# Kernel tuning notes

Measured on AMD Instinct MI355X. Metric: run time of the kernel, lower is better.

Reference implementation:

```python
import jax, jax.numpy as jnp
import numpy as np

N_NODES = 100_000
N_EDGES = 1_000_000
N_GRAPHS = 2048
F_IN, N_HEADS, HEAD_DIM = 128, 2, 32
NEG_SLOPE = 0.2


def seg_softmax(logits, seg, num):
    # numerically stable scatter-softmax over segments (leading axis)
    m = jax.ops.segment_max(logits, seg, num_segments=num)
    e = jnp.exp(logits - m[seg])
    s = jax.ops.segment_sum(e, seg, num_segments=num)
    return e / s[seg]


def setup_inputs() -> dict:
    key = jax.random.key(0)
    ks = jax.random.split(key, 10)
    HC = N_HEADS * HEAD_DIM
    x = jax.random.normal(ks[0], (N_NODES, F_IN), jnp.float32)
    edge_index = jax.random.randint(ks[1], (2, N_EDGES), 0, N_NODES, jnp.int32)
    batch = jnp.sort(jax.random.randint(ks[2], (N_NODES,), 0, N_GRAPHS, jnp.int32))
    sc_in = 1.0 / np.sqrt(F_IN)
    sc_hc = 1.0 / np.sqrt(HC)
    W_l = jax.random.normal(ks[3], (F_IN, HC), jnp.float32) * sc_in
    W_r = jax.random.normal(ks[4], (F_IN, HC), jnp.float32) * sc_in
    att = jax.random.normal(ks[5], (N_HEADS, HEAD_DIM), jnp.float32) * (1.0 / np.sqrt(HEAD_DIM))
    bias = jnp.zeros((HC,), jnp.float32)
    w_rel = jax.random.normal(ks[6], (HC,), jnp.float32) * sc_hc
    w_root = jax.random.normal(ks[7], (HC,), jnp.float32) * sc_hc
    b_score = jnp.zeros((1,), jnp.float32)
    return {"x": x, "edge_index": edge_index, "batch": batch, "W_l": W_l,
            "W_r": W_r, "att": att, "bias": bias, "w_rel": w_rel,
            "w_root": w_root, "b_score": b_score}


def reference(x, edge_index, batch, W_l, W_r, att, bias, w_rel, w_root, b_score):
    N = x.shape[0]
    H, C = att.shape
    src, dst = edge_index[0], edge_index[1]
    # --- GATv2Conv (add_self_loops=True, concat heads, negative_slope=0.2) ---
    loop = jnp.arange(N, dtype=src.dtype)
    s = jnp.concatenate([src, loop])  # source j
    d = jnp.concatenate([dst, loop])  # target i
    xl = (x @ W_l).reshape(N, H, C)   # lin_l -> source features
    xr = (x @ W_r).reshape(N, H, C)   # lin_r -> target features
    e = jax.nn.leaky_relu(xl[s] + xr[d], NEG_SLOPE)       # [E', H, C]
    logits = jnp.einsum('ehc,hc->eh', e, att)              # [E', H]
    alpha = seg_softmax(logits, d, N)                      # softmax over incoming edges per target
    h = jax.ops.segment_sum(xl[s] * alpha[:, :, None], d, num_segments=N)
    h = h.reshape(N, H * C) + bias                         # conv output (data.x)
    # --- SAGPooling(min_score=-1): softmax(GraphConv score) keeps all nodes ---
    aggr = jax.ops.segment_sum(h[src], dst, num_segments=N)  # GraphConv neighbor add-aggr
    score = aggr @ w_rel + h @ w_root + b_score              # [N]
    sm = seg_softmax(score, batch, N_GRAPHS)
    px = h * sm[:, None]
    # --- global_add_pool + global_mean_pool ---
    add = jax.ops.segment_sum(px, batch, num_segments=N_GRAPHS)
    cnt = jax.ops.segment_sum(jnp.ones((N,), px.dtype), batch, num_segments=N_GRAPHS)
    mean = add / jnp.maximum(cnt, 1.0)[:, None]
    return add + mean  # global_emb [N_GRAPHS, H*C]
```

## Files before the change

kernel.cpp:

```cpp
#include <hip/hip_runtime.h>
#include <hip/hip_bf16.h>

#define N_NODES 100000
#define N_EDGES 1000000
#define N_GRAPHS 2048
#define F_IN 128
#define NEG_SLOPE 0.2f
#define E_TOT (N_EDGES + N_NODES)
#define GEMM_BLOCKS 782
#define NODE_BLOCKS 391
#define NB 1563
#define EB 269
#define EB_PAD 272
#define CPW_BLOCKS 391

typedef short  bf16x8 __attribute__((ext_vector_type(8)));
typedef float  f32x16 __attribute__((ext_vector_type(16)));

__device__ __forceinline__ short f2bf(float f) {
    unsigned u = __float_as_uint(f);
    unsigned r = (u + 0x7fffu + ((u >> 16) & 1u)) >> 16;
    return (short)r;
}
__device__ __forceinline__ float bf2f(short h) {
    return __uint_as_float(((unsigned)(unsigned short)h) << 16);
}

template <int CTRL>
__device__ __forceinline__ float dpp_add(float x) {
    return x + __int_as_float(__builtin_amdgcn_update_dpp(
        0, __float_as_int(x), CTRL, 0xf, 0xf, true));
}
__device__ __forceinline__ float head_sum_bcast(float x) {
    x = dpp_add<0x111>(x);
    x = dpp_add<0x112>(x);
    x = dpp_add<0x114>(x);
    x = dpp_add<0x118>(x);
    x = dpp_add<0x142>(x);
    return __int_as_float(__builtin_amdgcn_ds_swizzle(__float_as_int(x), 0x03E0));
}
__device__ __forceinline__ float full_sum64(float x) {
    x = dpp_add<0x111>(x);
    x = dpp_add<0x112>(x);
    x = dpp_add<0x114>(x);
    x = dpp_add<0x118>(x);
    x = dpp_add<0x142>(x);
    x = dpp_add<0x143>(x);
    return x;
}
__device__ __forceinline__ float quad_sum(float x) {
    x = dpp_add<0xB1>(x);
    x = dpp_add<0x4E>(x);
    return x;
}

__global__ __launch_bounds__(256) void k_gemm_bhist(const float* __restrict__ x,
                                                    const float* __restrict__ Wl,
                                                    const float* __restrict__ Wr,
                                                    const int* __restrict__ ei,
                                                    float* __restrict__ xlr,
                                                    int* __restrict__ bhist) {
    __shared__ unsigned char smem[2 * 128 * 136 * 2];
    int tid = threadIdx.x;
    if (blockIdx.x >= GEMM_BLOCKS) {
        int* lh = (int*)smem;
        int b = blockIdx.x - GEMM_BLOCKS;
        for (int i = tid; i < NB; i += 256) lh[i] = 0;
        __syncthreads();
        int e0 = b * 4096;
#pragma unroll
        for (int j = 0; j < 16; ++j) {
            int e = e0 + j * 256 + tid;
            if (e < E_TOT) {
                int d = (e < N_EDGES) ? ei[N_EDGES + e] : (e - N_EDGES);
                atomicAdd(&lh[d >> 6], 1);
            }
        }
        __syncthreads();
        for (int i = tid; i < NB; i += 256)
            bhist[(size_t)i * EB_PAD + b] = lh[i];
        return;
    }
    typedef short wt_t[128][136];
    wt_t* wt = (wt_t*)smem;
    {
        int k  = tid >> 1;
        int cq = tid & 1;
        const float* Wsrc = cq ? Wr : Wl;
#pragma unroll
        for (int u = 0; u < 16; ++u) {
            int c0 = u * 4;
            float4 wv = *(const float4*)(Wsrc + (size_t)k * 64 + c0);
            float vv[4] = {wv.x, wv.y, wv.z, wv.w};
#pragma unroll
            for (int q = 0; q < 4; ++q) {
                int c = cq * 64 + c0 + q;
                short hi = f2bf(vv[q]);
                wt[0][c][k] = hi;
                wt[1][c][k] = f2bf(vv[q] - bf2f(hi));
            }
        }
    }
    __syncthreads();
    int lane = tid & 63, w = tid >> 6;
    int m = lane & 31, half = lane >> 5;
    int row = blockIdx.x * 128 + w * 32 + m;
    bool rv = row < N_NODES;
    const float* xrow = x + (size_t)(rv ? row : 0) * F_IN;
    f32x16 acc[4];
#pragma unroll
    for (int t = 0; t < 4; ++t)
#pragma unroll
        for (int i = 0; i < 16; ++i) acc[t][i] = 0.f;

#pragma unroll
    for (int kt = 0; kt < 8; ++kt) {
        int kb = kt * 16 + half * 8;
        float4 xa = rv ? *(const float4*)(xrow + kb)
                       : make_float4(0.f, 0.f, 0.f, 0.f);
        float4 xb = rv ? *(const float4*)(xrow + kb + 4)
                       : make_float4(0.f, 0.f, 0.f, 0.f);
        float xs[8] = {xa.x, xa.y, xa.z, xa.w, xb.x, xb.y, xb.z, xb.w};
        bf16x8 ahi, alo;
#pragma unroll
        for (int j = 0; j < 8; ++j) {
            short hi = f2bf(xs[j]);
            ahi[j] = hi;
            alo[j] = f2bf(xs[j] - bf2f(hi));
        }
#pragma unroll
        for (int t = 0; t < 4; ++t) {
            int n = t * 32 + m;
            bf16x8 bhi = *(const bf16x8*)&wt[0][n][kb];
            bf16x8 blo = *(const bf16x8*)&wt[1][n][kb];
            acc[t] = __builtin_amdgcn_mfma_f32_32x32x16_bf16(ahi, bhi, acc[t], 0, 0, 0);
            acc[t] = __builtin_amdgcn_mfma_f32_32x32x16_bf16(ahi, blo, acc[t], 0, 0, 0);
            acc[t] = __builtin_amdgcn_mfma_f32_32x32x16_bf16(alo, bhi, acc[t], 0, 0, 0);
        }
    }
    int r0 = blockIdx.x * 128 + w * 32 + 4 * half;
#pragma unroll
    for (int t = 0; t < 4; ++t)
#pragma unroll
        for (int reg = 0; reg < 16; ++reg) {
            int rr = r0 + (reg & 3) + 8 * (reg >> 2);
            if (rr < N_NODES)
                xlr[(size_t)rr * 128 + t * 32 + m] = acc[t][reg];
        }
}

__global__ __launch_bounds__(256) void k_colprefix_bounds(int* __restrict__ bhist,
                                                          int* __restrict__ colsum,
                                                          const int* __restrict__ batch,
                                                          int* __restrict__ start) {
    if (blockIdx.x < CPW_BLOCKS) {
        int wv = blockIdx.x * 4 + (threadIdx.x >> 6);
        if (wv >= NB) return;
        int lane = threadIdx.x & 63;
        int* row = bhist + (size_t)wv * EB_PAD;
        int carry = 0;
        for (int base = 0; base < EB; base += 64) {
            int idx = base + lane;
            int v = (idx < EB) ? row[idx] : 0;
            int inc = v;
#pragma unroll
            for (int o = 1; o < 64; o <<= 1) {
                int t = __shfl_up(inc, o, 64);
                if (lane >= o) inc += t;
            }
            int tot = __shfl(inc, 63, 64);
            if (idx < EB) row[idx] = carry + inc - v;
            carry += tot;
        }
        if (lane == 0) colsum[wv] = carry;
    } else {
        int i = (blockIdx.x - CPW_BLOCKS) * 256 + threadIdx.x;
        if (i >= N_NODES) return;
        int bi = batch[i];
        int bp = (i == 0) ? -1 : batch[i - 1];
        for (int g = bp + 1; g <= bi; ++g) start[g] = i;
        if (i == N_NODES - 1)
            for (int g = bi + 1; g <= N_GRAPHS; ++g) start[g] = N_NODES;
    }
}

__global__ __launch_bounds__(256) void k_bscatter(const int* __restrict__ ei,
                                                  const int* __restrict__ bhist,
                                                  const int* __restrict__ colsum,
                                                  int* __restrict__ colbase,
                                                  int* __restrict__ bpack) {
    __shared__ int lh[NB];
    __shared__ int cb[NB + 1];
    __shared__ int sctmp[256];
    int tid = threadIdx.x, b = blockIdx.x;
    {
        int v[7]; int s = 0;
#pragma unroll
        for (int k = 0; k < 7; ++k) {
            int idx = tid * 7 + k;
            v[k] = (idx < NB) ? colsum[idx] : 0;
            s += v[k];
        }
        sctmp[tid] = s; __syncthreads();
        for (int off = 1; off < 256; off <<= 1) {
            int xv = (tid >= off) ? sctmp[tid - off] : 0;
            __syncthreads();
            sctmp[tid] += xv;
            __syncthreads();
        }
        int run = sctmp[tid] - s;
#pragma unroll
        for (int k = 0; k < 7; ++k) {
            int idx = tid * 7 + k;
            if (idx <= NB) cb[idx] = run;
            run += v[k];
        }
    }
    for (int i = tid; i < NB; i += 256) lh[i] = 0;
    __syncthreads();
    if (b == 0)
        for (int i = tid; i <= NB; i += 256) colbase[i] = cb[i];
    int e0 = b * 4096;
#pragma unroll
    for (int j = 0; j < 16; ++j) {
        int e = e0 + j * 256 + tid;
        if (e < E_TOT) {
            int s, d;
            if (e < N_EDGES) { s = ei[e]; d = ei[N_EDGES + e]; }
            else             { s = d = e - N_EDGES; }
            int bk = d >> 6;
            int lr = atomicAdd(&lh[bk], 1);
            int pos = cb[bk] + bhist[(size_t)bk * EB_PAD + b] + lr;
            bpack[pos] = s | ((d & 63) << 17);
        }
    }
}

__global__ __launch_bounds__(256) void k_fine(const int* __restrict__ bpack,
                                              const int* __restrict__ colbase,
                                              int* __restrict__ rowptr,
                                              int* __restrict__ sorted_src) {
    __shared__ int fcnt[64];
    __shared__ int foff[64];
    int i = blockIdx.x, tid = threadIdx.x;
    int cb0 = colbase[i], cb1 = colbase[i + 1];
    if (tid < 64) fcnt[tid] = 0;
    __syncthreads();
    for (int e = cb0 + tid; e < cb1; e += 256)
        atomicAdd(&fcnt[bpack[e] >> 17], 1);
    __syncthreads();
    if (tid < 64) {
        int v = fcnt[tid];
        int inc = v;
#pragma unroll
        for (int o = 1; o < 64; o <<= 1) {
            int t = __shfl_up(inc, o, 64);
            if (tid >= o) inc += t;
        }
        int excl = inc - v;
        foff[tid] = excl;
        int node = i * 64 + tid;
        if (node <= N_NODES) rowptr[node] = cb0 + excl;
    }
    __syncthreads();
    for (int e = cb0 + tid; e < cb1; e += 256) {
        int w = bpack[e];
        int lr = atomicAdd(&foff[w >> 17], 1);
        sorted_src[cb0 + lr] = w & 131071;
    }
}

__global__ __launch_bounds__(256) void k_gat(const float* __restrict__ xlr,
                                             const int* __restrict__ rowptr,
                                             const int* __restrict__ sorted_src,
                                             const float* __restrict__ att,
                                             const float* __restrict__ bias,
                                             const float* __restrict__ w_rel,
                                             const float* __restrict__ w_root,
                                             float* __restrict__ hfeat,
                                             float* __restrict__ tbuf,
                                             float* __restrict__ rbuf) {
    int lane = threadIdx.x & 63;
    int du = __builtin_amdgcn_readfirstlane(blockIdx.x * 4 + (threadIdx.x >> 6));
    if (du >= N_NODES) return;
    float xr_l  = xlr[(size_t)du * 128 + 64 + lane];
    float att_l = att[lane];
    int j0 = __builtin_amdgcn_readfirstlane(rowptr[du]);
    int j1 = __builtin_amdgcn_readfirstlane(rowptr[du + 1]);
    float wsum = 0.f, acc = 0.f;
    int jc = j0;
    float xv[8];
    {
        int jj = jc + (lane & 7);
        if (jj > j1 - 1) jj = j1 - 1;
        int sv = sorted_src[jj];
#pragma unroll
        for (int i = 0; i < 8; ++i) {
            int s = __builtin_amdgcn_readlane(sv, i);
            xv[i] = (xlr + (size_t)(unsigned)s * 128)[lane];
        }
    }
    while (true) {
        int n = j1 - jc;
        int jn = jc + 8;
        bool more = jn < j1;
        float xvn[8];
        if (more) {
            int jj = jn + (lane & 7);
            if (jj > j1 - 1) jj = j1 - 1;
            int sv = sorted_src[jj];
#pragma unroll
            for (int i = 0; i < 8; ++i) {
                int s = __builtin_amdgcn_readlane(sv, i);
                xvn[i] = (xlr + (size_t)(unsigned)s * 128)[lane];
            }
        }
        float p[8];
#pragma unroll
        for (int i = 0; i < 8; ++i) {
            float v = xv[i] + xr_l;
            v = (v > 0.f) ? v : NEG_SLOPE * v;
            p[i] = v * att_l;
        }
#pragma unroll
        for (int i = 0; i < 8; ++i)
            p[i] = head_sum_bcast(p[i]);
        if (n >= 8) {
#pragma unroll
            for (int i = 0; i < 8; ++i) {
                float w = __expf(p[i]);
                wsum += w;
                acc += w * xv[i];
            }
        } else {
#pragma unroll
            for (int i = 0; i < 8; ++i) {
                float w = (i < n) ? __expf(p[i]) : 0.f;
                wsum += w;
                acc += w * xv[i];
            }
        }
        if (!more) break;
        jc = jn;
#pragma unroll
        for (int i = 0; i < 8; ++i) xv[i] = xvn[i];
    }
    float h = acc / wsum + bias[lane];
    hfeat[(size_t)du * 64 + lane] = h;
    float a = full_sum64(h * w_rel[lane]);
    float b = full_sum64(h * w_root[lane]);
    if (lane == 63) { tbuf[du] = a; rbuf[du] = b; }
}

__global__ __launch_bounds__(256) void k_pool(const int* __restrict__ rowptr,
                                              const int* __restrict__ sorted_src,
                                              const float* __restrict__ t,
                                              const float* __restrict__ r,
                                              const float* __restrict__ b_score,
                                              float* __restrict__ score,
                                              const float* __restrict__ h,
                                              const int* __restrict__ start,
                                              float* __restrict__ out) {
    __shared__ float sh[4];
    __shared__ float shacc[4][64];
    int g = blockIdx.x;
    int tid = threadIdx.x, w = tid >> 6, lane = tid & 63;
    int n0 = start[g], n1 = start[g + 1];
    int cnt = n1 - n0;
    if (cnt <= 0) { if (tid < 64) out[(size_t)g * 64 + tid] = 0.f; return; }
    float bsc = b_score[0];
    for (int base = n0; base < n1; base += 64) {
        int i = base + (tid >> 2);
        float sum = 0.f;
        int jj0 = 0, jj1 = 0;
        if (i < n1) { jj0 = rowptr[i]; jj1 = rowptr[i + 1]; }
        for (int j = jj0 + (tid & 3); j < jj1; j += 4)
            sum += t[sorted_src[j]];
        sum = quad_sum(sum);
        if (i < n1 && (tid & 3) == 0)
            score[i] = sum - t[i] + r[i] + bsc;
    }
    __syncthreads();
    float m = -1e30f;
    for (int i = n0 + tid; i < n1; i += 256) m = fmaxf(m, score[i]);
#pragma unroll
    for (int o = 32; o; o >>= 1) m = fmaxf(m, __shfl_xor(m, o, 64));
    if (lane == 0) sh[w] = m;
    __syncthreads();
    m = fmaxf(fmaxf(sh[0], sh[1]), fmaxf(sh[2], sh[3]));
    __syncthreads();
    float ssum = 0.f;
    for (int i = n0 + tid; i < n1; i += 256) {
        float e = __expf(score[i] - m);
        score[i] = e;
        ssum += e;
    }
#pragma unroll
    for (int o = 32; o; o >>= 1) ssum += __shfl_xor(ssum, o, 64);
    if (lane == 0) sh[w] = ssum;
    __syncthreads();
    ssum = sh[0] + sh[1] + sh[2] + sh[3];
    float acc = 0.f;
    for (int i = n0 + w; i < n1; i += 4)
        acc += score[i] * h[(size_t)i * 64 + lane];
    shacc[w][lane] = acc;
    __syncthreads();
    if (w == 0) {
        float tot = shacc[0][lane] + shacc[1][lane] + shacc[2][lane] + shacc[3][lane];
        out[(size_t)g * 64 + lane] = tot * (1.f + 1.f / (float)cnt) / ssum;
    }
}

extern "C" void kernel_launch(void* const* d_in, const int* in_sizes, int n_in,
                              void* d_out, int out_size, void* d_ws, size_t ws_size,
                              hipStream_t stream) {
    const float* x      = (const float*)d_in[0];
    const int*   ei     = (const int*)d_in[1];
    const int*   batch  = (const int*)d_in[2];
    const float* Wl     = (const float*)d_in[3];
    const float* Wr     = (const float*)d_in[4];
    const float* att    = (const float*)d_in[5];
    const float* bias   = (const float*)d_in[6];
    const float* w_rel  = (const float*)d_in[7];
    const float* w_root = (const float*)d_in[8];
    const float* b_sc   = (const float*)d_in[9];

    char* ws = (char*)d_ws;
    size_t off = 0;
    auto alloc = [&](size_t bytes) { void* p = ws + off; off += (bytes + 255) & ~255ull; return p; };
    float* xlr        = (float*)alloc((size_t)N_NODES * 128 * 4);
    float* hfeat      = (float*)alloc((size_t)N_NODES * 64 * 4);
    int*   bhist      = (int*)hfeat;
    int*   bpack      = (int*)  alloc((size_t)E_TOT * 4);
    int*   sorted_src = (int*)  alloc((size_t)E_TOT * 4);
    int*   rowptr     = (int*)  alloc((size_t)(N_NODES + 1) * 4);
    int*   colsum     = (int*)  alloc((size_t)NB * 4);
    int*   colbase    = (int*)  alloc((size_t)(NB + 1) * 4);
    float* tbuf       = (float*)alloc((size_t)N_NODES * 4);
    float* rbuf       = (float*)alloc((size_t)N_NODES * 4);
    float* score      = (float*)alloc((size_t)N_NODES * 4);
    int*   start      = (int*)  alloc((size_t)(N_GRAPHS + 1) * 4);

    k_gemm_bhist      <<<GEMM_BLOCKS + EB, 256, 0, stream>>>(x, Wl, Wr, ei, xlr, bhist);
    k_colprefix_bounds<<<CPW_BLOCKS + NODE_BLOCKS, 256, 0, stream>>>(bhist, colsum, batch, start);
    k_bscatter        <<<EB, 256, 0, stream>>>(ei, bhist, colsum, colbase, bpack);
    k_fine            <<<NB, 256, 0, stream>>>(bpack, colbase, rowptr, sorted_src);
    k_gat             <<<(N_NODES + 3) / 4, 256, 0, stream>>>(xlr, rowptr, sorted_src, att, bias,
                                                              w_rel, w_root, hfeat, tbuf, rbuf);
    k_pool            <<<N_GRAPHS, 256, 0, stream>>>(rowptr, sorted_src, tbuf, rbuf, b_sc,
                                                     score, hfeat, start, (float*)d_out);
}
```

Measured before the change: 238.0 us.

## Store source features in bf16 and process 8 edges per wave in parallel lanes

Measured after the change: 229.8 us. 3.4% less time.

```diff
diff --git a/kernel.cpp b/kernel.cpp
--- a/kernel.cpp
+++ b/kernel.cpp
@@ -31,14 +31,6 @@
     return x + __int_as_float(__builtin_amdgcn_update_dpp(
         0, __float_as_int(x), CTRL, 0xf, 0xf, true));
 }
-__device__ __forceinline__ float head_sum_bcast(float x) {
-    x = dpp_add<0x111>(x);
-    x = dpp_add<0x112>(x);
-    x = dpp_add<0x114>(x);
-    x = dpp_add<0x118>(x);
-    x = dpp_add<0x142>(x);
-    return __int_as_float(__builtin_amdgcn_ds_swizzle(__float_as_int(x), 0x03E0));
-}
 __device__ __forceinline__ float full_sum64(float x) {
     x = dpp_add<0x111>(x);
     x = dpp_add<0x112>(x);
@@ -58,7 +50,8 @@
                                                     const float* __restrict__ Wl,
                                                     const float* __restrict__ Wr,
                                                     const int* __restrict__ ei,
-                                                    float* __restrict__ xlr,
+                                                    float* __restrict__ xr,
+                                                    short* __restrict__ xlb,
                                                     int* __restrict__ bhist) {
     __shared__ unsigned char smem[2 * 128 * 136 * 2];
     int tid = threadIdx.x;
@@ -144,8 +137,12 @@
 #pragma unroll
         for (int reg = 0; reg < 16; ++reg) {
             int rr = r0 + (reg & 3) + 8 * (reg >> 2);
-            if (rr < N_NODES)
-                xlr[(size_t)rr * 128 + t * 32 + m] = acc[t][reg];
+            if (rr < N_NODES) {
+                if (t < 2)
+                    xlb[(size_t)rr * 64 + t * 32 + m] = f2bf(acc[t][reg]);
+                else
+                    xr[(size_t)rr * 64 + (t - 2) * 32 + m] = acc[t][reg];
+            }
         }
 }
 
@@ -270,7 +267,8 @@
     }
 }
 
-__global__ __launch_bounds__(256) void k_gat(const float* __restrict__ xlr,
+__global__ __launch_bounds__(256) void k_gat(const short* __restrict__ xlb,
+                                             const float* __restrict__ xr,
                                              const int* __restrict__ rowptr,
                                              const int* __restrict__ sorted_src,
                                              const float* __restrict__ att,
@@ -283,72 +281,72 @@
     int lane = threadIdx.x & 63;
     int du = __builtin_amdgcn_readfirstlane(blockIdx.x * 4 + (threadIdx.x >> 6));
     if (du >= N_NODES) return;
-    float xr_l  = xlr[(size_t)du * 128 + 64 + lane];
-    float att_l = att[lane];
+    int grp = lane >> 3, sub = lane & 7;
+    float xr8[8], att8[8];
+    {
+        float4 a = *(const float4*)(xr + (size_t)du * 64 + sub * 8);
+        float4 b = *(const float4*)(xr + (size_t)du * 64 + sub * 8 + 4);
+        xr8[0]=a.x; xr8[1]=a.y; xr8[2]=a.z; xr8[3]=a.w;
+        xr8[4]=b.x; xr8[5]=b.y; xr8[6]=b.z; xr8[7]=b.w;
+        float4 c = *(const float4*)(att + sub * 8);
+        float4 d = *(const float4*)(att + sub * 8 + 4);
+        att8[0]=c.x; att8[1]=c.y; att8[2]=c.z; att8[3]=c.w;
+        att8[4]=d.x; att8[5]=d.y; att8[6]=d.z; att8[7]=d.w;
+    }
     int j0 = __builtin_amdgcn_readfirstlane(rowptr[du]);
     int j1 = __builtin_amdgcn_readfirstlane(rowptr[du + 1]);
-    float wsum = 0.f, acc = 0.f;
-    int jc = j0;
-    float xv[8];
-    {
-        int jj = jc + (lane & 7);
+    float wsum = 0.f;
+    float acc8[8] = {0.f,0.f,0.f,0.f,0.f,0.f,0.f,0.f};
+    for (int jc = j0; jc < j1; jc += 8) {
+        int n = j1 - jc;
+        int jj = jc + grp;
         if (jj > j1 - 1) jj = j1 - 1;
-        int sv = sorted_src[jj];
-#pragma unroll
-        for (int i = 0; i < 8; ++i) {
-            int s = __builtin_amdgcn_readlane(sv, i);
-            xv[i] = (xlr + (size_t)(unsigned)s * 128)[lane];
-        }
-    }
-    while (true) {
-        int n = j1 - jc;
-        int jn = jc + 8;
-        bool more = jn < j1;
-        float xvn[8];
-        if (more) {
-            int jj = jn + (lane & 7);
-            if (jj > j1 - 1) jj = j1 - 1;
-            int sv = sorted_src[jj];
-#pragma unroll
-            for (int i = 0; i < 8; ++i) {
-                int s = __builtin_amdgcn_readlane(sv, i);
-                xvn[i] = (xlr + (size_t)(unsigned)s * 128)[lane];
-            }
-        }
-        float p[8];
-#pragma unroll
-        for (int i = 0; i < 8; ++i) {
-            float v = xv[i] + xr_l;
-            v = (v > 0.f) ? v : NEG_SLOPE * v;
-            p[i] = v * att_l;
-        }
-#pragma unroll
-        for (int i = 0; i < 8; ++i)
-            p[i] = head_sum_bcast(p[i]);
-        if (n >= 8) {
-#pragma unroll
-            for (int i = 0; i < 8; ++i) {
-                float w = __expf(p[i]);
-                wsum += w;
-                acc += w * xv[i];
-            }
-        } else {
-#pragma unroll
-            for (int i = 0; i < 8; ++i) {
-                float w = (i < n) ? __expf(p[i]) : 0.f;
-                wsum += w;
-                acc += w * xv[i];
-            }
-        }
-        if (!more) break;
-        jc = jn;
-#pragma unroll
-        for (int i = 0; i < 8; ++i) xv[i] = xvn[i];
-    }
-    float h = acc / wsum + bias[lane];
-    hfeat[(size_t)du * 64 + lane] = h;
-    float a = full_sum64(h * w_rel[lane]);
-    float b = full_sum64(h * w_root[lane]);
+        int s = sorted_src[jj];
+        bf16x8 xb = *(const bf16x8*)(xlb + (size_t)(unsigned)s * 64 + sub * 8);
+        float xv8[8];
+#pragma unroll
+        for (int j = 0; j < 8; ++j) xv8[j] = bf2f(xb[j]);
+        float p = 0.f;
+#pragma unroll
+        for (int j = 0; j < 8; ++j) {
+            float v = xv8[j] + xr8[j];
+            v = fmaxf(v, NEG_SLOPE * v);
+            p += v * att8[j];
+        }
+        p = quad_sum(p);
+        float w = __expf(p);
+        if (grp >= n) w = 0.f;
+        wsum += w;
+#pragma unroll
+        for (int j = 0; j < 8; ++j) acc8[j] += w * xv8[j];
+    }
+    wsum += __shfl_xor(wsum, 8, 64);
+    wsum += __shfl_xor(wsum, 16, 64);
+    wsum += __shfl_xor(wsum, 32, 64);
+#pragma unroll
+    for (int j = 0; j < 8; ++j) {
+        acc8[j] += __shfl_xor(acc8[j], 8, 64);
+        acc8[j] += __shfl_xor(acc8[j], 16, 64);
+        acc8[j] += __shfl_xor(acc8[j], 32, 64);
+    }
+    float h8[8];
+#pragma unroll
+    for (int j = 0; j < 8; ++j)
+        h8[j] = acc8[j] / wsum + bias[sub * 8 + j];
+    if (grp == 0) {
+        float4 s0 = make_float4(h8[0], h8[1], h8[2], h8[3]);
+        float4 s1 = make_float4(h8[4], h8[5], h8[6], h8[7]);
+        *(float4*)(hfeat + (size_t)du * 64 + sub * 8)     = s0;
+        *(float4*)(hfeat + (size_t)du * 64 + sub * 8 + 4) = s1;
+    }
+    float a = 0.f, b = 0.f;
+#pragma unroll
+    for (int j = 0; j < 8; ++j) {
+        a += h8[j] * w_rel[sub * 8 + j];
+        b += h8[j] * w_root[sub * 8 + j];
+    }
+    a = full_sum64(a) * 0.125f;
+    b = full_sum64(b) * 0.125f;
     if (lane == 63) { tbuf[du] = a; rbuf[du] = b; }
 }
 
@@ -428,7 +426,8 @@
     char* ws = (char*)d_ws;
     size_t off = 0;
     auto alloc = [&](size_t bytes) { void* p = ws + off; off += (bytes + 255) & ~255ull; return p; };
-    float* xlr        = (float*)alloc((size_t)N_NODES * 128 * 4);
+    float* xr         = (float*)alloc((size_t)N_NODES * 64 * 4);
+    short* xlb        = (short*)alloc((size_t)N_NODES * 64 * 2);
     float* hfeat      = (float*)alloc((size_t)N_NODES * 64 * 4);
     int*   bhist      = (int*)hfeat;
     int*   bpack      = (int*)  alloc((size_t)E_TOT * 4);
@@ -441,11 +440,11 @@
     float* score      = (float*)alloc((size_t)N_NODES * 4);
     int*   start      = (int*)  alloc((size_t)(N_GRAPHS + 1) * 4);
 
-    k_gemm_bhist      <<<GEMM_BLOCKS + EB, 256, 0, stream>>>(x, Wl, Wr, ei, xlr, bhist);
+    k_gemm_bhist      <<<GEMM_BLOCKS + EB, 256, 0, stream>>>(x, Wl, Wr, ei, xr, xlb, bhist);
     k_colprefix_bounds<<<CPW_BLOCKS + NODE_BLOCKS, 256, 0, stream>>>(bhist, colsum, batch, start);
     k_bscatter        <<<EB, 256, 0, stream>>>(ei, bhist, colsum, colbase, bpack);
     k_fine            <<<NB, 256, 0, stream>>>(bpack, colbase, rowptr, sorted_src);
-    k_gat             <<<(N_NODES + 3) / 4, 256, 0, stream>>>(xlr, rowptr, sorted_src, att, bias,
+    k_gat             <<<(N_NODES + 3) / 4, 256, 0, stream>>>(xlb, xr, rowptr, sorted_src, att, bias,
                                                               w_rel, w_root, hfeat, tbuf, rbuf);
     k_pool            <<<N_GRAPHS, 256, 0, stream>>>(rowptr, sorted_src, tbuf, rbuf, b_sc,
                                                      score, hfeat, start, (float*)d_out);
```
